# Optimization experiments

Hardware: AMD Instinct MI355X
Metric: run time of the kernel (lower is better)

## Reference

```python
import jax, jax.numpy as jnp
import numpy as np

K = 5  # kernel_size hardcoded in Net
PAD = (K - 1) // 2


def _patches(x):
    # x: [B, C, H, W] -> [B, C, K*K, H, W] (zero-padded sliding windows, like nn.Unfold)
    B, C, H, W = x.shape
    xp = jnp.pad(x, ((0, 0), (0, 0), (PAD, PAD), (PAD, PAD)))
    return jnp.stack([xp[:, :, i:i + H, j:j + W]
                      for i in range(K) for j in range(K)], axis=2)


def setup_inputs() -> dict:
    key = jax.random.key(0)
    k1, k2, k3 = jax.random.split(key, 3)
    x = jax.random.uniform(k1, (16, 1, 512, 512), dtype=jnp.float32)
    noise_var = jax.random.uniform(k2, (1,), dtype=jnp.float32)
    noise_bias = jax.random.uniform(k3, (1,), dtype=jnp.float32)
    return {"x": x, "noise_var": noise_var, "noise_bias": noise_bias}


def reference(x, noise_var, noise_bias):
    p = _patches(x)                          # [B, C, 25, H, W]
    s_var = jnp.var(p, axis=2, ddof=1)       # torch.var is unbiased by default
    mid = jnp.median(p, axis=2)              # odd window -> exact middle element
    y = x - noise_var / (s_var + 1e-10) * (x - mid + noise_bias)
    return jax.nn.relu(y)
```

## Files before the change

kernel.cpp:

```cpp
#include <hip/hip_runtime.h>

#define PAD 2
#define PX 4
#define WROWS 4
#define TSX 64
#define LTW 68
#define LTH (WROWS + 2 * PAD)
#define SLICE (LTH * LTW)
#define NCHUNK (SLICE / 4)

typedef float v4f __attribute__((ext_vector_type(4)));

typedef __attribute__((address_space(1))) const void ga_void;
typedef __attribute__((address_space(3))) void ls_void;

__device__ __forceinline__ float min3f(float a, float b, float c) {
    return fminf(fminf(a, b), c);
}
__device__ __forceinline__ float max3f(float a, float b, float c) {
    return fmaxf(fmaxf(a, b), c);
}
__device__ __forceinline__ float med3f(float a, float b, float c) {
    return fmaxf(fminf(a, b), fminf(fmaxf(a, b), c));
}

#define CE(a, b) { float _lo = fminf(a, b), _hi = fmaxf(a, b); (a) = _lo; (b) = _hi; }

#define MED9(q0, q1, q2, q3, q4, q5, q6, q7, q8) \
    CE(q1, q2) CE(q4, q5) CE(q7, q8) \
    CE(q0, q1) CE(q3, q4) CE(q6, q7) \
    CE(q1, q2) CE(q4, q5) CE(q7, q8) \
    CE(q0, q3) CE(q5, q8) CE(q4, q7) \
    CE(q3, q6) CE(q1, q4) CE(q2, q5) \
    CE(q4, q7) CE(q4, q2) CE(q6, q4) \
    CE(q4, q2)

__global__ __launch_bounds__(64, 5) void denoise_median5_kernel(
    const float* __restrict__ x,
    const float* __restrict__ noise_var_p,
    const float* __restrict__ noise_bias_p,
    float* __restrict__ out,
    int H, int W)
{
    __shared__ float lds[SLICE];

    const float noise_var  = noise_var_p[0];
    const float noise_bias = noise_bias_p[0];

    const int lane = threadIdx.x;

    const int b      = blockIdx.z;
    const int tile_x = blockIdx.x * TSX;
    const int wy     = blockIdx.y * WROWS;
    const int gy0    = wy - PAD;
    const int gx0    = tile_x - PAD;

    const float* __restrict__ img = x + (size_t)b * H * W;
    float* __restrict__ ldsbase = &lds[0];

    const bool interior = (blockIdx.x >= 1) && (blockIdx.x <= gridDim.x - 2) &&
                          (wy >= PAD) && (wy <= H - LTH + PAD);

    if (interior) {
        const float* gbase = img + (size_t)gy0 * W + gx0;
        #pragma unroll
        for (int batch = 0; batch < 2; ++batch) {
            const int chunk = batch * 64 + lane;
            const int row = chunk / 17;
            const int cc  = chunk - row * 17;
            const float* gsrc = gbase + (size_t)row * W + cc * 4;
            __builtin_amdgcn_global_load_lds((ga_void*)gsrc,
                                             (ls_void*)(ldsbase + batch * 256),
                                             16, 0, 0);
        }
        if (lane < NCHUNK - 128) {
            const int chunk = 128 + lane;
            const int row = chunk / 17;
            const int cc  = chunk - row * 17;
            const float* gsrc = gbase + (size_t)row * W + cc * 4;
            __builtin_amdgcn_global_load_lds((ga_void*)gsrc,
                                             (ls_void*)(ldsbase + 512),
                                             16, 0, 0);
        }
        asm volatile("s_waitcnt vmcnt(0)" ::: "memory");
        __builtin_amdgcn_sched_barrier(0);
    } else {
        for (int i = lane; i < SLICE; i += 64) {
            const int ly = i / LTW;
            const int lx = i - ly * LTW;
            const int gy = gy0 + ly;
            const int gx = gx0 + lx;
            float v = 0.0f;
            if ((unsigned)gy < (unsigned)H && (unsigned)gx < (unsigned)W)
                v = img[(size_t)gy * W + gx];
            ldsbase[i] = v;
        }
        asm volatile("s_waitcnt lgkmcnt(0)" ::: "memory");
        __builtin_amdgcn_sched_barrier(0);
    }

    const int lx16 = lane & 15;
    const int lrow = lane >> 4;

    v4f A[5], Dq[5];
    #pragma unroll
    for (int r = 0; r < 5; ++r) {
        A[r]  = *(const v4f*)&ldsbase[(lrow + r) * LTW + lx16 * 4];
        Dq[r] = *(const v4f*)&ldsbase[(lrow + r) * LTW + lx16 * 4 + 4];
    }

    v4f SA = ((A[0] + A[1]) + (A[2] + A[3])) + A[4];
    v4f SD = ((Dq[0] + Dq[1]) + (Dq[2] + Dq[3])) + Dq[4];
    v4f QA = A[0] * A[0];
    v4f QD = Dq[0] * Dq[0];
    #pragma unroll
    for (int r = 1; r < 5; ++r) { QA = A[r] * A[r] + QA; QD = Dq[r] * Dq[r] + QD; }

    const float s8[8] = {SA.x, SA.y, SA.z, SA.w, SD.x, SD.y, SD.z, SD.w};
    const float q8[8] = {QA.x, QA.y, QA.z, QA.w, QD.x, QD.y, QD.z, QD.w};

    float sum5[PX], sq5[PX];
    sum5[0] = ((s8[0] + s8[1]) + (s8[2] + s8[3])) + s8[4];
    sq5[0]  = ((q8[0] + q8[1]) + (q8[2] + q8[3])) + q8[4];
    #pragma unroll
    for (int p = 1; p < PX; ++p) {
        sum5[p] = sum5[p - 1] - s8[p - 1] + s8[p + 4];
        sq5[p]  = sq5[p - 1]  - q8[p - 1] + q8[p + 4];
    }

    const float center[PX] = {A[2].z, A[2].w, Dq[2].x, Dq[2].y};

    float c[8][5];
    #pragma unroll
    for (int r = 0; r < 5; ++r) {
        c[0][r] = A[r].x;  c[1][r] = A[r].y;  c[2][r] = A[r].z;  c[3][r] = A[r].w;
        c[4][r] = Dq[r].x; c[5][r] = Dq[r].y; c[6][r] = Dq[r].z; c[7][r] = Dq[r].w;
    }
    #pragma unroll
    for (int k = 0; k < 8; ++k) {
        const float a1 = fminf(c[k][0], c[k][1]), a2 = fmaxf(c[k][0], c[k][1]);
        const float b1 = fminf(c[k][2], c[k][3]), b2 = fmaxf(c[k][2], c[k][3]);
        const float cc = c[k][4];
        const float t1 = fminf(a2, b2), t3 = fmaxf(a1, b1);
        const float M  = fmaxf(a2, b2), m  = fminf(a1, b1);
        c[k][0] = fminf(m, cc);
        c[k][4] = fmaxf(M, cc);
        c[k][2] = med3f(t1, t3, cc);
        c[k][3] = max3f(t1, fminf(cc, M), t3);
        c[k][1] = min3f(t3, fmaxf(cc, m), t1);
    }

    float4 res;
    float* resp = (float*)&res;

    #pragma unroll
    for (int p = 0; p < PX; ++p) {
        float A1, A2, B1, B2, B3, C1, C2, C3, D1, D2, D3, E1, E2;
        {
            const float a1 = fminf(c[p][0], c[p+1][0]), a2 = fmaxf(c[p][0], c[p+1][0]);
            const float b1 = fminf(c[p+2][0], c[p+3][0]), b2 = fmaxf(c[p+2][0], c[p+3][0]);
            const float cc = c[p+4][0];
            const float M = fmaxf(a2, b2), t1 = fminf(a2, b2), t3 = fmaxf(a1, b1);
            A2 = fmaxf(M, cc);
            A1 = max3f(t1, fminf(cc, M), t3);
        }
        {
            const float a1 = fminf(c[p][1], c[p+1][1]), a2 = fmaxf(c[p][1], c[p+1][1]);
            const float b1 = fminf(c[p+2][1], c[p+3][1]), b2 = fmaxf(c[p+2][1], c[p+3][1]);
            const float cc = c[p+4][1];
            const float M = fmaxf(a2, b2), t1 = fminf(a2, b2), t3 = fmaxf(a1, b1);
            B3 = fmaxf(M, cc);
            B2 = max3f(t1, fminf(cc, M), t3);
            B1 = med3f(t1, t3, cc);
        }
        {
            const float a1 = fminf(c[p][2], c[p+1][2]), a2 = fmaxf(c[p][2], c[p+1][2]);
            const float b1 = fminf(c[p+2][2], c[p+3][2]), b2 = fmaxf(c[p+2][2], c[p+3][2]);
            const float cc = c[p+4][2];
            const float M = fmaxf(a2, b2), m = fminf(a1, b1);
            const float t1 = fminf(a2, b2), t3 = fmaxf(a1, b1);
            C2 = med3f(t1, t3, cc);
            C3 = max3f(t1, fminf(cc, M), t3);
            C1 = min3f(t3, fmaxf(cc, m), t1);
        }
        {
            const float a1 = fminf(c[p][3], c[p+1][3]), a2 = fmaxf(c[p][3], c[p+1][3]);
            const float b1 = fminf(c[p+2][3], c[p+3][3]), b2 = fmaxf(c[p+2][3], c[p+3][3]);
            const float cc = c[p+4][3];
            const float m = fminf(a1, b1), t1 = fminf(a2, b2), t3 = fmaxf(a1, b1);
            D1 = fminf(m, cc);
            D2 = min3f(t3, fmaxf(cc, m), t1);
            D3 = med3f(t1, t3, cc);
        }
        {
            const float a1 = fminf(c[p][4], c[p+1][4]), a2 = fmaxf(c[p][4], c[p+1][4]);
            const float b1 = fminf(c[p+2][4], c[p+3][4]), b2 = fmaxf(c[p+2][4], c[p+3][4]);
            const float cc = c[p+4][4];
            const float m = fminf(a1, b1), t1 = fminf(a2, b2), t3 = fmaxf(a1, b1);
            E1 = fminf(m, cc);
            E2 = min3f(t3, fmaxf(cc, m), t1);
        }

        const float mn1 = fminf(B3, D3);
        const float mn2 = fminf(C3, E2);
        const float mx1 = fmaxf(B1, D1);
        const float mx2 = fmaxf(A1, C1);

        float q0 = mx2, q1 = A2, q2 = B2, q3 = C2, q4 = D2,
              q5 = E1, q6 = mx1, q7 = mn1, q8 = mn2;
        MED9(q0, q1, q2, q3, q4, q5, q6, q7, q8);
        const float mid = q4;

        const float sum = sum5[p];
        const float sq  = sq5[p];
        const float mean = sum * (1.0f / 25.0f);
        float var = (sq - sum * mean) * (1.0f / 24.0f);
        var = fmaxf(var, 0.0f);

        const float xc = center[p];
        const float rr = __builtin_amdgcn_rcpf(var + 1e-10f);
        float y = xc - noise_var * rr * (xc - mid + noise_bias);
        resp[p] = fmaxf(y, 0.0f);
    }

    const int orow = wy + lrow;
    const int ox   = tile_x + lx16 * PX;
    *(float4*)&out[((size_t)b * H + orow) * W + ox] = res;
}

extern "C" void kernel_launch(void* const* d_in, const int* in_sizes, int n_in,
                              void* d_out, int out_size, void* d_ws, size_t ws_size,
                              hipStream_t stream)
{
    const float* x  = (const float*)d_in[0];
    const float* nv = (const float*)d_in[1];
    const float* nb = (const float*)d_in[2];
    float* out = (float*)d_out;

    const int H = 512, W = 512;
    const int B = in_sizes[0] / (H * W);

    dim3 block(64, 1, 1);
    dim3 grid(W / TSX, H / WROWS, B);
    denoise_median5_kernel<<<grid, block, 0, stream>>>(x, nv, nb, out, H, W);
}
```

Measured before the change: 32.80 us.

## Process two row tiles per block with double-buffered async LDS loads

Each workgroup now handles two vertically adjacent 4-row tiles. It issues the async global-to-LDS loads for both tiles up front into separate LDS buffers, waits only for the first tile's loads, and computes it while the second tile's loads are still in flight. The grid is halved in y and the occupancy hint drops from 5 to 4 waves to make room for the doubled LDS and registers. The aim is to hide global load latency behind compute, at the cost of fewer workgroups and lower occupancy.

```diff
diff --git a/kernel.cpp b/kernel.cpp
--- a/kernel.cpp
+++ b/kernel.cpp
@@ -3,6 +3,7 @@
 #define PAD 2
 #define PX 4
 #define WROWS 4
+#define NT 2
 #define TSX 64
 #define LTW 68
 #define LTH (WROWS + 2 * PAD)
@@ -35,197 +36,238 @@
     CE(q4, q7) CE(q4, q2) CE(q6, q4) \
     CE(q4, q2)
 
-__global__ __launch_bounds__(64, 5) void denoise_median5_kernel(
+__global__ __launch_bounds__(64, 4) void denoise_median5_kernel(
     const float* __restrict__ x,
     const float* __restrict__ noise_var_p,
     const float* __restrict__ noise_bias_p,
     float* __restrict__ out,
     int H, int W)
 {
-    __shared__ float lds[SLICE];
+    __shared__ float lds[NT * SLICE];
 
     const float noise_var  = noise_var_p[0];
     const float noise_bias = noise_bias_p[0];
 
     const int lane = threadIdx.x;
-
     const int b      = blockIdx.z;
     const int tile_x = blockIdx.x * TSX;
-    const int wy     = blockIdx.y * WROWS;
-    const int gy0    = wy - PAD;
+    const int wy0    = blockIdx.y * (WROWS * NT);
+    const int wy1    = wy0 + WROWS;
     const int gx0    = tile_x - PAD;
 
     const float* __restrict__ img = x + (size_t)b * H * W;
-    float* __restrict__ ldsbase = &lds[0];
-
-    const bool interior = (blockIdx.x >= 1) && (blockIdx.x <= gridDim.x - 2) &&
-                          (wy >= PAD) && (wy <= H - LTH + PAD);
-
-    if (interior) {
-        const float* gbase = img + (size_t)gy0 * W + gx0;
+    float* __restrict__ buf0 = &lds[0];
+    float* __restrict__ buf1 = &lds[SLICE];
+
+    const bool okx  = (blockIdx.x >= 1) && (blockIdx.x <= gridDim.x - 2);
+    const bool int0 = okx && (wy0 >= PAD) && (wy0 <= H - LTH + PAD);
+    const bool int1 = okx && (wy1 >= PAD) && (wy1 <= H - LTH + PAD);
+
+    if (int0) {
+        const float* gbase = img + (size_t)(wy0 - PAD) * W + gx0;
         #pragma unroll
         for (int batch = 0; batch < 2; ++batch) {
             const int chunk = batch * 64 + lane;
             const int row = chunk / 17;
             const int cc  = chunk - row * 17;
-            const float* gsrc = gbase + (size_t)row * W + cc * 4;
-            __builtin_amdgcn_global_load_lds((ga_void*)gsrc,
-                                             (ls_void*)(ldsbase + batch * 256),
-                                             16, 0, 0);
+            __builtin_amdgcn_global_load_lds((ga_void*)(gbase + (size_t)row * W + cc * 4),
+                                             (ls_void*)(buf0 + batch * 256), 16, 0, 0);
         }
         if (lane < NCHUNK - 128) {
             const int chunk = 128 + lane;
             const int row = chunk / 17;
             const int cc  = chunk - row * 17;
-            const float* gsrc = gbase + (size_t)row * W + cc * 4;
-            __builtin_amdgcn_global_load_lds((ga_void*)gsrc,
-                                             (ls_void*)(ldsbase + 512),
-                                             16, 0, 0);
-        }
-        asm volatile("s_waitcnt vmcnt(0)" ::: "memory");
-        __builtin_amdgcn_sched_barrier(0);
+            __builtin_amdgcn_global_load_lds((ga_void*)(gbase + (size_t)row * W + cc * 4),
+                                             (ls_void*)(buf0 + 512), 16, 0, 0);
+        }
     } else {
         for (int i = lane; i < SLICE; i += 64) {
             const int ly = i / LTW;
             const int lx = i - ly * LTW;
-            const int gy = gy0 + ly;
+            const int gy = wy0 - PAD + ly;
             const int gx = gx0 + lx;
             float v = 0.0f;
             if ((unsigned)gy < (unsigned)H && (unsigned)gx < (unsigned)W)
                 v = img[(size_t)gy * W + gx];
-            ldsbase[i] = v;
-        }
-        asm volatile("s_waitcnt lgkmcnt(0)" ::: "memory");
-        __builtin_amdgcn_sched_barrier(0);
+            buf0[i] = v;
+        }
+    }
+
+    if (int1) {
+        const float* gbase = img + (size_t)(wy1 - PAD) * W + gx0;
+        #pragma unroll
+        for (int batch = 0; batch < 2; ++batch) {
+            const int chunk = batch * 64 + lane;
+            const int row = chunk / 17;
+            const int cc  = chunk - row * 17;
+            __builtin_amdgcn_global_load_lds((ga_void*)(gbase + (size_t)row * W + cc * 4),
+                                             (ls_void*)(buf1 + batch * 256), 16, 0, 0);
+        }
+        if (lane < NCHUNK - 128) {
+            const int chunk = 128 + lane;
+            const int row = chunk / 17;
+            const int cc  = chunk - row * 17;
+            __builtin_amdgcn_global_load_lds((ga_void*)(gbase + (size_t)row * W + cc * 4),
+                                             (ls_void*)(buf1 + 512), 16, 0, 0);
+        }
+    } else {
+        for (int i = lane; i < SLICE; i += 64) {
+            const int ly = i / LTW;
+            const int lx = i - ly * LTW;
+            const int gy = wy1 - PAD + ly;
+            const int gx = gx0 + lx;
+            float v = 0.0f;
+            if ((unsigned)gy < (unsigned)H && (unsigned)gx < (unsigned)W)
+                v = img[(size_t)gy * W + gx];
+            buf1[i] = v;
+        }
     }
 
     const int lx16 = lane & 15;
     const int lrow = lane >> 4;
 
-    v4f A[5], Dq[5];
-    #pragma unroll
-    for (int r = 0; r < 5; ++r) {
-        A[r]  = *(const v4f*)&ldsbase[(lrow + r) * LTW + lx16 * 4];
-        Dq[r] = *(const v4f*)&ldsbase[(lrow + r) * LTW + lx16 * 4 + 4];
-    }
-
-    v4f SA = ((A[0] + A[1]) + (A[2] + A[3])) + A[4];
-    v4f SD = ((Dq[0] + Dq[1]) + (Dq[2] + Dq[3])) + Dq[4];
-    v4f QA = A[0] * A[0];
-    v4f QD = Dq[0] * Dq[0];
-    #pragma unroll
-    for (int r = 1; r < 5; ++r) { QA = A[r] * A[r] + QA; QD = Dq[r] * Dq[r] + QD; }
-
-    const float s8[8] = {SA.x, SA.y, SA.z, SA.w, SD.x, SD.y, SD.z, SD.w};
-    const float q8[8] = {QA.x, QA.y, QA.z, QA.w, QD.x, QD.y, QD.z, QD.w};
-
-    float sum5[PX], sq5[PX];
-    sum5[0] = ((s8[0] + s8[1]) + (s8[2] + s8[3])) + s8[4];
-    sq5[0]  = ((q8[0] + q8[1]) + (q8[2] + q8[3])) + q8[4];
-    #pragma unroll
-    for (int p = 1; p < PX; ++p) {
-        sum5[p] = sum5[p - 1] - s8[p - 1] + s8[p + 4];
-        sq5[p]  = sq5[p - 1]  - q8[p - 1] + q8[p + 4];
-    }
-
-    const float center[PX] = {A[2].z, A[2].w, Dq[2].x, Dq[2].y};
-
-    float c[8][5];
-    #pragma unroll
-    for (int r = 0; r < 5; ++r) {
-        c[0][r] = A[r].x;  c[1][r] = A[r].y;  c[2][r] = A[r].z;  c[3][r] = A[r].w;
-        c[4][r] = Dq[r].x; c[5][r] = Dq[r].y; c[6][r] = Dq[r].z; c[7][r] = Dq[r].w;
-    }
-    #pragma unroll
-    for (int k = 0; k < 8; ++k) {
-        const float a1 = fminf(c[k][0], c[k][1]), a2 = fmaxf(c[k][0], c[k][1]);
-        const float b1 = fminf(c[k][2], c[k][3]), b2 = fmaxf(c[k][2], c[k][3]);
-        const float cc = c[k][4];
-        const float t1 = fminf(a2, b2), t3 = fmaxf(a1, b1);
-        const float M  = fmaxf(a2, b2), m  = fminf(a1, b1);
-        c[k][0] = fminf(m, cc);
-        c[k][4] = fmaxf(M, cc);
-        c[k][2] = med3f(t1, t3, cc);
-        c[k][3] = max3f(t1, fminf(cc, M), t3);
-        c[k][1] = min3f(t3, fmaxf(cc, m), t1);
-    }
-
-    float4 res;
-    float* resp = (float*)&res;
-
-    #pragma unroll
-    for (int p = 0; p < PX; ++p) {
-        float A1, A2, B1, B2, B3, C1, C2, C3, D1, D2, D3, E1, E2;
-        {
-            const float a1 = fminf(c[p][0], c[p+1][0]), a2 = fmaxf(c[p][0], c[p+1][0]);
-            const float b1 = fminf(c[p+2][0], c[p+3][0]), b2 = fmaxf(c[p+2][0], c[p+3][0]);
-            const float cc = c[p+4][0];
-            const float M = fmaxf(a2, b2), t1 = fminf(a2, b2), t3 = fmaxf(a1, b1);
-            A2 = fmaxf(M, cc);
-            A1 = max3f(t1, fminf(cc, M), t3);
-        }
-        {
-            const float a1 = fminf(c[p][1], c[p+1][1]), a2 = fmaxf(c[p][1], c[p+1][1]);
-            const float b1 = fminf(c[p+2][1], c[p+3][1]), b2 = fmaxf(c[p+2][1], c[p+3][1]);
-            const float cc = c[p+4][1];
-            const float M = fmaxf(a2, b2), t1 = fminf(a2, b2), t3 = fmaxf(a1, b1);
-            B3 = fmaxf(M, cc);
-            B2 = max3f(t1, fminf(cc, M), t3);
-            B1 = med3f(t1, t3, cc);
-        }
-        {
-            const float a1 = fminf(c[p][2], c[p+1][2]), a2 = fmaxf(c[p][2], c[p+1][2]);
-            const float b1 = fminf(c[p+2][2], c[p+3][2]), b2 = fmaxf(c[p+2][2], c[p+3][2]);
-            const float cc = c[p+4][2];
-            const float M = fmaxf(a2, b2), m = fminf(a1, b1);
+    auto compute_tile = [&](const float* __restrict__ ldsbase, int wy) {
+        v4f A[5], Dq[5];
+        #pragma unroll
+        for (int r = 0; r < 5; ++r) {
+            A[r]  = *(const v4f*)&ldsbase[(lrow + r) * LTW + lx16 * 4];
+            Dq[r] = *(const v4f*)&ldsbase[(lrow + r) * LTW + lx16 * 4 + 4];
+        }
+
+        v4f SA = ((A[0] + A[1]) + (A[2] + A[3])) + A[4];
+        v4f SD = ((Dq[0] + Dq[1]) + (Dq[2] + Dq[3])) + Dq[4];
+        v4f QA = A[0] * A[0];
+        v4f QD = Dq[0] * Dq[0];
+        #pragma unroll
+        for (int r = 1; r < 5; ++r) { QA = A[r] * A[r] + QA; QD = Dq[r] * Dq[r] + QD; }
+
+        const float s8[8] = {SA.x, SA.y, SA.z, SA.w, SD.x, SD.y, SD.z, SD.w};
+        const float q8[8] = {QA.x, QA.y, QA.z, QA.w, QD.x, QD.y, QD.z, QD.w};
+
+        float sum5[PX], sq5[PX];
+        sum5[0] = ((s8[0] + s8[1]) + (s8[2] + s8[3])) + s8[4];
+        sq5[0]  = ((q8[0] + q8[1]) + (q8[2] + q8[3])) + q8[4];
+        #pragma unroll
+        for (int p = 1; p < PX; ++p) {
+            sum5[p] = sum5[p - 1] - s8[p - 1] + s8[p + 4];
+            sq5[p]  = sq5[p - 1]  - q8[p - 1] + q8[p + 4];
+        }
+
+        const float center[PX] = {A[2].z, A[2].w, Dq[2].x, Dq[2].y};
+
+        float c[8][5];
+        #pragma unroll
+        for (int r = 0; r < 5; ++r) {
+            c[0][r] = A[r].x;  c[1][r] = A[r].y;  c[2][r] = A[r].z;  c[3][r] = A[r].w;
+            c[4][r] = Dq[r].x; c[5][r] = Dq[r].y; c[6][r] = Dq[r].z; c[7][r] = Dq[r].w;
+        }
+        #pragma unroll
+        for (int k = 0; k < 8; ++k) {
+            const float a1 = fminf(c[k][0], c[k][1]), a2 = fmaxf(c[k][0], c[k][1]);
+            const float b1 = fminf(c[k][2], c[k][3]), b2 = fmaxf(c[k][2], c[k][3]);
+            const float cc = c[k][4];
             const float t1 = fminf(a2, b2), t3 = fmaxf(a1, b1);
-            C2 = med3f(t1, t3, cc);
-            C3 = max3f(t1, fminf(cc, M), t3);
-            C1 = min3f(t3, fmaxf(cc, m), t1);
-        }
-        {
-            const float a1 = fminf(c[p][3], c[p+1][3]), a2 = fmaxf(c[p][3], c[p+1][3]);
-            const float b1 = fminf(c[p+2][3], c[p+3][3]), b2 = fmaxf(c[p+2][3], c[p+3][3]);
-            const float cc = c[p+4][3];
-            const float m = fminf(a1, b1), t1 = fminf(a2, b2), t3 = fmaxf(a1, b1);
-            D1 = fminf(m, cc);
-            D2 = min3f(t3, fmaxf(cc, m), t1);
-            D3 = med3f(t1, t3, cc);
-        }
-        {
-            const float a1 = fminf(c[p][4], c[p+1][4]), a2 = fmaxf(c[p][4], c[p+1][4]);
-            const float b1 = fminf(c[p+2][4], c[p+3][4]), b2 = fmaxf(c[p+2][4], c[p+3][4]);
-            const float cc = c[p+4][4];
-            const float m = fminf(a1, b1), t1 = fminf(a2, b2), t3 = fmaxf(a1, b1);
-            E1 = fminf(m, cc);
-            E2 = min3f(t3, fmaxf(cc, m), t1);
-        }
-
-        const float mn1 = fminf(B3, D3);
-        const float mn2 = fminf(C3, E2);
-        const float mx1 = fmaxf(B1, D1);
-        const float mx2 = fmaxf(A1, C1);
-
-        float q0 = mx2, q1 = A2, q2 = B2, q3 = C2, q4 = D2,
-              q5 = E1, q6 = mx1, q7 = mn1, q8 = mn2;
-        MED9(q0, q1, q2, q3, q4, q5, q6, q7, q8);
-        const float mid = q4;
-
-        const float sum = sum5[p];
-        const float sq  = sq5[p];
-        const float mean = sum * (1.0f / 25.0f);
-        float var = (sq - sum * mean) * (1.0f / 24.0f);
-        var = fmaxf(var, 0.0f);
-
-        const float xc = center[p];
-        const float rr = __builtin_amdgcn_rcpf(var + 1e-10f);
-        float y = xc - noise_var * rr * (xc - mid + noise_bias);
-        resp[p] = fmaxf(y, 0.0f);
-    }
-
-    const int orow = wy + lrow;
-    const int ox   = tile_x + lx16 * PX;
-    *(float4*)&out[((size_t)b * H + orow) * W + ox] = res;
+            const float M  = fmaxf(a2, b2), m  = fminf(a1, b1);
+            c[k][0] = fminf(m, cc);
+            c[k][4] = fmaxf(M, cc);
+            c[k][2] = med3f(t1, t3, cc);
+            c[k][3] = max3f(t1, fminf(cc, M), t3);
+            c[k][1] = min3f(t3, fmaxf(cc, m), t1);
+        }
+
+        float4 res;
+        float* resp = (float*)&res;
+
+        #pragma unroll
+        for (int p = 0; p < PX; ++p) {
+            float A1, A2, B1, B2, B3, C1, C2, C3, D1, D2, D3, E1, E2;
+            {
+                const float a1 = fminf(c[p][0], c[p+1][0]), a2 = fmaxf(c[p][0], c[p+1][0]);
+                const float b1 = fminf(c[p+2][0], c[p+3][0]), b2 = fmaxf(c[p+2][0], c[p+3][0]);
+                const float cc = c[p+4][0];
+                const float M = fmaxf(a2, b2), t1 = fminf(a2, b2), t3 = fmaxf(a1, b1);
+                A2 = fmaxf(M, cc);
+                A1 = max3f(t1, fminf(cc, M), t3);
+            }
+            {
+                const float a1 = fminf(c[p][1], c[p+1][1]), a2 = fmaxf(c[p][1], c[p+1][1]);
+                const float b1 = fminf(c[p+2][1], c[p+3][1]), b2 = fmaxf(c[p+2][1], c[p+3][1]);
+                const float cc = c[p+4][1];
+                const float M = fmaxf(a2, b2), t1 = fminf(a2, b2), t3 = fmaxf(a1, b1);
+                B3 = fmaxf(M, cc);
+                B2 = max3f(t1, fminf(cc, M), t3);
+                B1 = med3f(t1, t3, cc);
+            }
+            {
+                const float a1 = fminf(c[p][2], c[p+1][2]), a2 = fmaxf(c[p][2], c[p+1][2]);
+                const float b1 = fminf(c[p+2][2], c[p+3][2]), b2 = fmaxf(c[p+2][2], c[p+3][2]);
+                const float cc = c[p+4][2];
+                const float M = fmaxf(a2, b2), m = fminf(a1, b1);
+                const float t1 = fminf(a2, b2), t3 = fmaxf(a1, b1);
+                C2 = med3f(t1, t3, cc);
+                C3 = max3f(t1, fminf(cc, M), t3);
+                C1 = min3f(t3, fmaxf(cc, m), t1);
+            }
+            {
+                const float a1 = fminf(c[p][3], c[p+1][3]), a2 = fmaxf(c[p][3], c[p+1][3]);
+                const float b1 = fminf(c[p+2][3], c[p+3][3]), b2 = fmaxf(c[p+2][3], c[p+3][3]);
+                const float cc = c[p+4][3];
+                const float m = fminf(a1, b1), t1 = fminf(a2, b2), t3 = fmaxf(a1, b1);
+                D1 = fminf(m, cc);
+                D2 = min3f(t3, fmaxf(cc, m), t1);
+                D3 = med3f(t1, t3, cc);
+            }
+            {
+                const float a1 = fminf(c[p][4], c[p+1][4]), a2 = fmaxf(c[p][4], c[p+1][4]);
+                const float b1 = fminf(c[p+2][4], c[p+3][4]), b2 = fmaxf(c[p+2][4], c[p+3][4]);
+                const float cc = c[p+4][4];
+                const float m = fminf(a1, b1), t1 = fminf(a2, b2), t3 = fmaxf(a1, b1);
+                E1 = fminf(m, cc);
+                E2 = min3f(t3, fmaxf(cc, m), t1);
+            }
+
+            const float mn1 = fminf(B3, D3);
+            const float mn2 = fminf(C3, E2);
+            const float mx1 = fmaxf(B1, D1);
+            const float mx2 = fmaxf(A1, C1);
+
+            float q0 = mx2, q1 = A2, q2 = B2, q3 = C2, q4 = D2,
+                  q5 = E1, q6 = mx1, q7 = mn1, q8 = mn2;
+            MED9(q0, q1, q2, q3, q4, q5, q6, q7, q8);
+            const float mid = q4;
+
+            const float sum = sum5[p];
+            const float sq  = sq5[p];
+            const float mean = sum * (1.0f / 25.0f);
+            float var = (sq - sum * mean) * (1.0f / 24.0f);
+            var = fmaxf(var, 0.0f);
+
+            const float xc = center[p];
+            const float rr = __builtin_amdgcn_rcpf(var + 1e-10f);
+            float y = xc - noise_var * rr * (xc - mid + noise_bias);
+            resp[p] = fmaxf(y, 0.0f);
+        }
+
+        const int orow = wy + lrow;
+        const int ox   = tile_x + lx16 * PX;
+        *(float4*)&out[((size_t)b * H + orow) * W + ox] = res;
+    };
+
+    if (int0 && int1) {
+        asm volatile("s_waitcnt vmcnt(3)" ::: "memory");
+    } else {
+        asm volatile("s_waitcnt vmcnt(0) lgkmcnt(0)" ::: "memory");
+    }
+    __builtin_amdgcn_sched_barrier(0);
+    compute_tile(buf0, wy0);
+
+    if (int1) {
+        asm volatile("s_waitcnt vmcnt(1) lgkmcnt(0)" ::: "memory");
+    } else {
+        asm volatile("s_waitcnt lgkmcnt(0)" ::: "memory");
+    }
+    __builtin_amdgcn_sched_barrier(0);
+    compute_tile(buf1, wy1);
 }
 
 extern "C" void kernel_launch(void* const* d_in, const int* in_sizes, int n_in,
@@ -241,6 +283,6 @@
     const int B = in_sizes[0] / (H * W);
 
     dim3 block(64, 1, 1);
-    dim3 grid(W / TSX, H / WROWS, B);
+    dim3 grid(W / TSX, H / (WROWS * NT), B);
     denoise_median5_kernel<<<grid, block, 0, stream>>>(x, nv, nb, out, H, W);
 }
```

Result: slower. 34.80 us (+6.1%).
